# Kernel tuning notes

Hardware: AMD Instinct MI355X
Metric: run time of the kernel (lower is better)

The kernel has to match this reference:

```python
import jax, jax.numpy as jnp
import numpy as np

B, S, D = 8, 2048, 64
H = 128


def setup_inputs() -> dict:
    key = jax.random.key(0)
    k = jax.random.split(key, 5)
    X = jax.random.normal(k[0], (B, S, D), dtype=jnp.float32)
    Wi = jax.random.normal(k[1], (H, D), dtype=jnp.float32)          # init_layer weight, std=1
    bi = jax.random.normal(k[2], (H,), dtype=jnp.float32)            # init_layer bias, std=1
    Wa = jax.random.normal(k[3], (H * H, D + 1), dtype=jnp.float32) / jnp.sqrt(H)  # vf_A, std=1/sqrt(H)
    Wb = jax.random.normal(k[4], (H, D + 1), dtype=jnp.float32)      # vf_B, std=1
    return {"X": X, "Wi": Wi, "bi": bi, "Wa": Wa, "Wb": Wb}


def reference(X, Wi, bi, Wa, Wb):
    b, s, d = X.shape
    dt = 1.0 / (s - 1)
    # inp: time channel (constant dt) concatenated with scaled input -> [b, s, d+1]
    inp = jnp.concatenate([jnp.full((b, s, 1), dt, dtype=X.dtype), X * dt], axis=-1)
    y0 = X[:, 0] @ Wi.T + bi                       # [b, H]
    Bs = jnp.einsum('bsk,hk->bsh', inp[:, 1:], Wb)  # [b, s-1, H]

    def step(y, xs):
        inp_t, b_t = xs                            # [b, d+1], [b, H]
        A = (inp_t @ Wa.T).reshape(b, H, H)        # per-step transition matrix
        y_new = y + jnp.einsum('bij,bj->bi', A, y) + b_t
        return y_new, y_new

    xs = (jnp.swapaxes(inp[:, 1:], 0, 1), jnp.swapaxes(Bs, 0, 1))  # time-major
    _, ys_rest = jax.lax.scan(step, y0, xs)        # [s-1, b, H]
    ys = jnp.concatenate([y0[:, None, :], jnp.swapaxes(ys_rest, 0, 1)], axis=1)
    return ys
```

## Files before the change

kernel.cpp:

```cpp
#include <hip/hip_runtime.h>
#include <hip/hip_fp16.h>


typedef _Float16 h8 __attribute__((ext_vector_type(8)));
typedef float v4f __attribute__((ext_vector_type(4)));
typedef unsigned int uint;

constexpr int B_ = 8, S_ = 2048, D_ = 64, H_ = 128;
constexpr int T_ = S_ - 1;
constexpr int KD = D_ + 1;
constexpr float DTC = 1.0f / 2047.0f;
constexpr int L_ = 8;
constexpr int LSH = 3;
constexpr int NC = 256;

__global__ __launch_bounds__(256) void k_prep_wa(const float* __restrict__ Wa,
                                                 _Float16* __restrict__ Wa16B,
                                                 float* __restrict__ Wa0) {
  int idx = blockIdx.x * 256 + threadIdx.x;
  int r = idx >> 6, kk = idx & 63;
  int rt = r >> 4, n = r & 15;
  int kb = kk >> 5, q = (kk >> 3) & 3, jj = kk & 7;
  float v = Wa[(size_t)r * KD + 1 + kk];
  Wa16B[((((size_t)rt * 2 + kb) * 4 + q) * 16 + n) * 8 + jj] = (_Float16)v;
  if (kk == 0) Wa0[r] = Wa[(size_t)r * KD];
}

__global__ __launch_bounds__(256) void k_prep_x(const float* __restrict__ X,
                                                _Float16* __restrict__ Xs16) {
  int idx = blockIdx.x * 256 + threadIdx.x;
  int bt = idx >> 6, d = idx & 63;
  int b = bt / T_, s = bt - b * T_;
  Xs16[(size_t)bt * 64 + d] = (_Float16)(X[((size_t)b * S_ + s + 1) * D_ + d] * DTC);
}

__global__ __launch_bounds__(128) void k_y0(const float* __restrict__ X,
                                            const float* __restrict__ Wi,
                                            const float* __restrict__ bi,
                                            float* __restrict__ out,
                                            float* __restrict__ ybound) {
  int b = blockIdx.x, h = threadIdx.x;
  __shared__ float xs[D_];
  if (h < D_) xs[h] = X[(size_t)b * S_ * D_ + h];
  __syncthreads();
  float acc = bi[h];
  const float* wr = Wi + h * D_;
#pragma unroll 8
  for (int d = 0; d < D_; d++) acc += xs[d] * wr[d];
  out[(size_t)b * S_ * H_ + h] = acc;
  if (ybound) ybound[(size_t)(b * NC + 0) * H_ + h] = acc;
}

__global__ __launch_bounds__(256) void k_bs(const float* __restrict__ X,
                                            const float* __restrict__ Wb,
                                            float* __restrict__ Bs) {
  __shared__ float wb_s[H_ * KD];
  __shared__ float xs[16][D_ + 4];
  int tid = threadIdx.x;
  int bt0 = blockIdx.x * 16;
  for (int i = tid; i < H_ * KD; i += 256) wb_s[i] = Wb[i];
  for (int i = tid; i < 16 * D_; i += 256) {
    int sl = i >> 6, d = i & 63;
    int btg = bt0 + sl;
    float v = 0.f;
    if (btg < B_ * T_) {
      int b = btg / T_, s = btg - b * T_;
      v = X[((size_t)b * S_ + s + 1) * D_ + d] * DTC;
    }
    xs[sl][d] = v;
  }
  __syncthreads();
  int h = tid & 127, sh = tid >> 7;
  const float* wrow = &wb_s[h * KD];
  for (int u = 0; u < 8; u++) {
    int sl = sh * 8 + u;
    int btg = bt0 + sl;
    if (btg >= B_ * T_) break;
    float acc = wrow[0] * DTC;
#pragma unroll 8
    for (int d = 0; d < D_; d++) acc += xs[sl][d] * wrow[1 + d];
    Bs[(size_t)btg * H_ + h] = acc;
  }
}

__global__ __launch_bounds__(256) void k_amat(const _Float16* __restrict__ Xs16,
                                              const _Float16* __restrict__ Wa16B,
                                              const float* __restrict__ Wa0,
                                              _Float16* __restrict__ A_sl,
                                              int c0, int scShift) {
  __shared__ _Float16 sb[32 * 528];
  int tid = threadIdx.x;
  int w = tid >> 6, lane = tid & 63;
  int n = lane & 15, q = lane >> 4;
  int rowbase = blockIdx.x * 32;
  int SCm = ((1 << scShift) << LSH) - 1;

  h8 af[2][2];
#pragma unroll
  for (int mi = 0; mi < 2; mi++) {
    int sidx = rowbase + mi * 16 + n;
    int b = sidx >> (scShift + LSH);
    int rem = sidx & SCm;
    int cc = rem >> LSH, l = rem & (L_ - 1);
    int s = (c0 + cc) * L_ + l;
    if (s >= T_) s = T_ - 1;
    size_t btg = (size_t)b * T_ + s;
#pragma unroll
    for (int kb = 0; kb < 2; kb++)
      af[mi][kb] = *(const h8*)(Xs16 + btg * 64 + kb * 32 + q * 8);
  }

  v4f acc[2][8];
#pragma unroll
  for (int nj = 0; nj < 8; nj++) {
    int ct_g = blockIdx.y * 32 + w * 8 + nj;
    float binit = DTC * Wa0[ct_g * 16 + n];
    h8 bf0 = *(const h8*)(Wa16B + ((((size_t)ct_g * 2 + 0) * 4 + q) * 16 + n) * 8);
    h8 bf1 = *(const h8*)(Wa16B + ((((size_t)ct_g * 2 + 1) * 4 + q) * 16 + n) * 8);
#pragma unroll
    for (int mi = 0; mi < 2; mi++) {
      v4f a;
      a[0] = binit; a[1] = binit; a[2] = binit; a[3] = binit;
      a = __builtin_amdgcn_mfma_f32_16x16x32_f16(af[mi][0], bf0, a, 0, 0, 0);
      a = __builtin_amdgcn_mfma_f32_16x16x32_f16(af[mi][1], bf1, a, 0, 0, 0);
      acc[mi][nj] = a;
    }
  }
#pragma unroll
  for (int mi = 0; mi < 2; mi++)
#pragma unroll
    for (int nj = 0; nj < 8; nj++)
#pragma unroll
      for (int reg = 0; reg < 4; reg++)
        sb[(mi * 16 + q * 4 + reg) * 528 + w * 128 + ((nj * 16 + n) ^ (q * 16))] =
            (_Float16)acc[mi][nj][reg];
  __syncthreads();
#pragma unroll
  for (int it = 0; it < 8; it++) {
    int idx = tid + it * 256;
    int t = idx >> 6, u4 = idx & 63;
    int qt = (t >> 2) & 3;
    uint4 val = *(const uint4*)&sb[t * 528 + ((u4 * 8) ^ (qt * 16))];
    *(uint4*)(A_sl + (size_t)(rowbase + t) * 16384 + blockIdx.y * 512 + u4 * 8) = val;
  }
}

__global__ __launch_bounds__(256) void k_pair(const _Float16* __restrict__ A_sl,
                                              const float* __restrict__ Bs,
                                              _Float16* __restrict__ P1,
                                              float* __restrict__ v1,
                                              int c0, int scShift) {
  __shared__ _Float16 A0t[128 * 136];
  __shared__ float bs0[128], bs1[128];
  int tid = threadIdx.x;
  int w = tid >> 6, lane = tid & 63;
  int n = lane & 15, q = lane >> 4;
  int chunk = blockIdx.x >> 2;
  int j = blockIdx.x & 3;
  int SC = 1 << scShift;
  int b = chunk >> scShift;
  int cc = chunk & (SC - 1);
  int c = c0 + cc;
  int t0 = c * L_ + 2 * j;
  int valid1 = (t0 + 1) < T_;
  const _Float16* A0 = A_sl + ((size_t)chunk * L_ + 2 * j) * 16384;
  const _Float16* A1 = A0 + 16384;

#pragma unroll
  for (int it = 0; it < 8; it++) {
    int idx = tid + it * 256;
    int rowl = idx & 127, c8 = (idx >> 7) * 8;
    uint4 pk = *(const uint4*)(A0 + rowl * 128 + c8);
    const _Float16* hp = (const _Float16*)&pk;
#pragma unroll
    for (int cx = 0; cx < 8; cx++) A0t[(c8 + cx) * 136 + rowl] = hp[cx];
  }
  if (tid < 128) {
    size_t bt0 = (size_t)b * T_ + t0;
    bs0[tid] = Bs[bt0 * 128 + tid];
    bs1[tid] = valid1 ? Bs[(bt0 + 1) * 128 + tid] : 0.f;
  }
  h8 idE, idO;
#pragma unroll
  for (int jj = 0; jj < 8; jj++) {
    idE[jj] = (_Float16)((q * 8 + jj == n) ? 1.f : 0.f);
    idO[jj] = (_Float16)((q * 8 + jj == 16 + n) ? 1.f : 0.f);
  }
  h8 af[2][4];
  if (valid1) {
#pragma unroll
    for (int mi = 0; mi < 2; mi++)
#pragma unroll
      for (int kb = 0; kb < 4; kb++)
        af[mi][kb] = *(const h8*)(A1 + ((2 * w + mi) * 16 + n) * 128 + kb * 32 + q * 8);
  } else {
#pragma unroll
    for (int mi = 0; mi < 2; mi++)
#pragma unroll
      for (int kb = 0; kb < 4; kb++)
#pragma unroll
        for (int z = 0; z < 8; z++) af[mi][kb][z] = (_Float16)0;
  }
  __syncthreads();

  v4f acc[2][8];
#pragma unroll
  for (int mi = 0; mi < 2; mi++)
#pragma unroll
    for (int nj = 0; nj < 8; nj++)
#pragma unroll
      for (int reg = 0; reg < 4; reg++) acc[mi][nj][reg] = 0.f;

#pragma unroll
  for (int nj = 0; nj < 8; nj++) {
    h8 bfr[4];
#pragma unroll
    for (int kb = 0; kb < 4; kb++)
      bfr[kb] = *(const h8*)&A0t[(nj * 16 + n) * 136 + kb * 32 + q * 8];
#pragma unroll
    for (int mi = 0; mi < 2; mi++) {
#pragma unroll
      for (int kb = 0; kb < 4; kb++)
        acc[mi][nj] = __builtin_amdgcn_mfma_f32_16x16x32_f16(af[mi][kb], bfr[kb], acc[mi][nj], 0, 0, 0);
      acc[mi][nj] = __builtin_amdgcn_mfma_f32_16x16x32_f16(
          af[mi][nj >> 1], (nj & 1) ? idO : idE, acc[mi][nj], 0, 0, 0);
    }
  }

  float dv0 = 0.f, dv1 = 0.f;
#pragma unroll
  for (int kb = 0; kb < 4; kb++) {
    float4 p0 = *(const float4*)&bs0[kb * 32 + q * 8];
    float4 p1 = *(const float4*)&bs0[kb * 32 + q * 8 + 4];
    float vk[8] = {p0.x, p0.y, p0.z, p0.w, p1.x, p1.y, p1.z, p1.w};
#pragma unroll
    for (int jj = 0; jj < 8; jj++) {
      dv0 += (float)af[0][kb][jj] * vk[jj];
      dv1 += (float)af[1][kb][jj] * vk[jj];
    }
  }
  dv0 += __shfl_xor(dv0, 16); dv0 += __shfl_xor(dv0, 32);
  dv1 += __shfl_xor(dv1, 16); dv1 += __shfl_xor(dv1, 32);
  if (q == 0) {
    float* v1g = v1 + (size_t)blockIdx.x * 128;
    int r0v = 2 * w * 16 + n, r1v = (2 * w + 1) * 16 + n;
    v1g[r0v] = bs0[r0v] + bs1[r0v] + dv0;
    v1g[r1v] = bs0[r1v] + bs1[r1v] + dv1;
  }

#pragma unroll
  for (int mi = 0; mi < 2; mi++) {
    int row0 = (2 * w + mi) * 16 + q * 4;
#pragma unroll
    for (int nj = 0; nj < 8; nj++) {
      int col = nj * 16 + n;
      union { uint2 u; _Float16 h[4]; } m2;
      m2.u = *(const uint2*)&A0t[col * 136 + row0];
#pragma unroll
      for (int reg = 0; reg < 4; reg++) acc[mi][nj][reg] += (float)m2.h[reg];
    }
  }
  __syncthreads();
#pragma unroll
  for (int mi = 0; mi < 2; mi++) {
    int row0 = (2 * w + mi) * 16 + q * 4;
#pragma unroll
    for (int nj = 0; nj < 8; nj++) {
      int col = nj * 16 + n;
#pragma unroll
      for (int reg = 0; reg < 4; reg++)
        A0t[(row0 + reg) * 136 + col] = (_Float16)acc[mi][nj][reg];
    }
  }
  __syncthreads();
  _Float16* Pg = P1 + (size_t)blockIdx.x * 16384;
#pragma unroll
  for (int it = 0; it < 8; it++) {
    int idx = tid + it * 256;
    int rowl = idx >> 4, ch = idx & 15;
    uint4 val = *(const uint4*)&A0t[rowl * 136 + ch * 8];
    *(uint4*)(Pg + rowl * 128 + ch * 8) = val;
  }
}

__global__ __launch_bounds__(256) void k_comp4(const _Float16* __restrict__ in_map,
                                               const float* __restrict__ in_v,
                                               _Float16* __restrict__ out_map,
                                               float* __restrict__ out_v) {
  __shared__ _Float16 Dt[128 * 136];
  __shared__ float v32[128];
  int tid = threadIdx.x;
  int w = tid >> 6, lane = tid & 63;
  int n = lane & 15, q = lane >> 4;
  size_t nbase = (size_t)blockIdx.x * 4;

  const _Float16* P0 = in_map + nbase * 16384;
#pragma unroll
  for (int it = 0; it < 8; it++) {
    int idx = tid + it * 256;
    int rowl = idx & 127, c8 = (idx >> 7) * 8;
    uint4 pk = *(const uint4*)(P0 + rowl * 128 + c8);
    const _Float16* hp = (const _Float16*)&pk;
#pragma unroll
    for (int cx = 0; cx < 8; cx++) Dt[(c8 + cx) * 136 + rowl] = hp[cx];
  }
  if (tid < 128) v32[tid] = in_v[nbase * 128 + tid];
  h8 idE, idO;
#pragma unroll
  for (int jj = 0; jj < 8; jj++) {
    idE[jj] = (_Float16)((q * 8 + jj == n) ? 1.f : 0.f);
    idO[jj] = (_Float16)((q * 8 + jj == 16 + n) ? 1.f : 0.f);
  }
  __syncthreads();

  v4f acc[2][8];
#pragma unroll
  for (int mi = 0; mi < 2; mi++) {
    int row0 = (2 * w + mi) * 16 + q * 4;
#pragma unroll
    for (int nj = 0; nj < 8; nj++) {
      int col = nj * 16 + n;
      union { uint2 u; _Float16 h[4]; } m2;
      m2.u = *(const uint2*)&Dt[col * 136 + row0];
#pragma unroll
      for (int reg = 0; reg < 4; reg++) acc[mi][nj][reg] = (float)m2.h[reg];
    }
  }

  int r0 = 2 * w * 16 + n, r1 = r0 + 16;
  for (int j = 1; j < 4; j++) {
    const _Float16* Pj = in_map + (nbase + j) * 16384;
    h8 af[2][4];
#pragma unroll
    for (int mi = 0; mi < 2; mi++)
#pragma unroll
      for (int kb = 0; kb < 4; kb++)
        af[mi][kb] = *(const h8*)(Pj + ((2 * w + mi) * 16 + n) * 128 + kb * 32 + q * 8);
#pragma unroll
    for (int nj = 0; nj < 8; nj++) {
      h8 bfr[4];
#pragma unroll
      for (int kb = 0; kb < 4; kb++)
        bfr[kb] = *(const h8*)&Dt[(nj * 16 + n) * 136 + kb * 32 + q * 8];
#pragma unroll
      for (int mi = 0; mi < 2; mi++) {
#pragma unroll
        for (int kb = 0; kb < 4; kb++)
          acc[mi][nj] = __builtin_amdgcn_mfma_f32_16x16x32_f16(af[mi][kb], bfr[kb], acc[mi][nj], 0, 0, 0);
        acc[mi][nj] = __builtin_amdgcn_mfma_f32_16x16x32_f16(
            af[mi][nj >> 1], (nj & 1) ? idO : idE, acc[mi][nj], 0, 0, 0);
      }
    }
    float dv0 = 0.f, dv1 = 0.f;
#pragma unroll
    for (int kb = 0; kb < 4; kb++) {
      float4 p0 = *(const float4*)&v32[kb * 32 + q * 8];
      float4 p1 = *(const float4*)&v32[kb * 32 + q * 8 + 4];
      float vk[8] = {p0.x, p0.y, p0.z, p0.w, p1.x, p1.y, p1.z, p1.w};
#pragma unroll
      for (int jj = 0; jj < 8; jj++) {
        dv0 += (float)af[0][kb][jj] * vk[jj];
        dv1 += (float)af[1][kb][jj] * vk[jj];
      }
    }
    dv0 += __shfl_xor(dv0, 16); dv0 += __shfl_xor(dv0, 32);
    dv1 += __shfl_xor(dv1, 16); dv1 += __shfl_xor(dv1, 32);
    float vold0 = v32[r0], vold1 = v32[r1];
    float vj0 = 0.f, vj1 = 0.f;
    if (q == 0) {
      vj0 = in_v[(nbase + j) * 128 + r0];
      vj1 = in_v[(nbase + j) * 128 + r1];
    }
    __syncthreads();
#pragma unroll
    for (int mi = 0; mi < 2; mi++) {
      int row0 = (2 * w + mi) * 16 + q * 4;
#pragma unroll
      for (int nj = 0; nj < 8; nj++) {
        int col = nj * 16 + n;
        union { _Float16 h[4]; uint2 u; } pk;
#pragma unroll
        for (int reg = 0; reg < 4; reg++) pk.h[reg] = (_Float16)acc[mi][nj][reg];
        *(uint2*)&Dt[col * 136 + row0] = pk.u;
      }
    }
    if (q == 0) {
      v32[r0] = vold0 + dv0 + vj0;
      v32[r1] = vold1 + dv1 + vj1;
    }
    __syncthreads();
  }
#pragma unroll
  for (int mi = 0; mi < 2; mi++) {
    int row0 = (2 * w + mi) * 16 + q * 4;
#pragma unroll
    for (int nj = 0; nj < 8; nj++) {
      int col = nj * 16 + n;
#pragma unroll
      for (int reg = 0; reg < 4; reg++)
        Dt[(row0 + reg) * 136 + col] = (_Float16)acc[mi][nj][reg];
    }
  }
  __syncthreads();
  _Float16* og = out_map + (size_t)blockIdx.x * 16384;
#pragma unroll
  for (int it = 0; it < 8; it++) {
    int idx = tid + it * 256;
    int rowl = idx >> 4, ch = idx & 15;
    uint4 val = *(const uint4*)&Dt[rowl * 136 + ch * 8];
    *(uint4*)(og + rowl * 128 + ch * 8) = val;
  }
  if (tid < 128) out_v[(size_t)blockIdx.x * 128 + tid] = v32[tid];
}

__global__ __launch_bounds__(256) void k_chainsuper(const _Float16* __restrict__ Sr,
                                                    const float* __restrict__ sv,
                                                    float* __restrict__ yb,
                                                    int c0, int scShift) {
  int b = blockIdx.x, tid = threadIdx.x;
  int NS = 1 << (scShift - 2);
  int i = tid >> 1, hh = tid & 1;
  __shared__ float ybuf[128];
  __shared__ float red[128];
  if (tid < 128) ybuf[tid] = yb[(size_t)(b * NC + c0) * 128 + tid];
  __syncthreads();

  uint4 arA[8], arB[8];
  float svA, svB;

#define LOADS(ar, svv, s)                                                            \
  {                                                                                  \
    const uint4* p = (const uint4*)(Sr + (size_t)(b * NS + (s)) * 16384 + i * 128 + hh * 64); \
    _Pragma("unroll")                                                                \
    for (int u = 0; u < 8; u++) ar[u] = p[u];                                        \
    svv = sv[(size_t)(b * NS + (s)) * 128 + i];                                      \
  }

#define STEPS(ar, svv, s)                                                            \
  {                                                                                  \
    float pt = 0.f;                                                                  \
    _Pragma("unroll")                                                                \
    for (int u = 0; u < 8; u++) {                                                    \
      union { uint4 v; _Float16 h[8]; } wv; wv.v = ar[u];                            \
      _Pragma("unroll")                                                              \
      for (int k = 0; k < 8; k++) pt += (float)wv.h[k] * ybuf[hh * 64 + u * 8 + k];  \
    }                                                                                \
    if (hh) red[i] = pt;                                                             \
    __syncthreads();                                                                 \
    if (!hh) {                                                                       \
      float yn = ybuf[i] + pt + red[i] + svv;                                        \
      int cg = c0 + 4 * ((s) + 1);                                                   \
      if (cg < NC) yb[(size_t)(b * NC + cg) * 128 + i] = yn;                         \
      ybuf[i] = yn;                                                                  \
    }                                                                                \
    __syncthreads();                                                                 \
  }

  LOADS(arA, svA, 0);
  int s = 0;
  for (; s + 1 < NS; s += 2) {
    LOADS(arB, svB, s + 1);
    STEPS(arA, svA, s);
    if (s + 2 < NS) LOADS(arA, svA, s + 2);
    STEPS(arB, svB, s + 1);
  }
  if (s < NS) STEPS(arA, svA, s);
#undef LOADS
#undef STEPS
}

__global__ __launch_bounds__(256) void k_fill(const _Float16* __restrict__ Mr,
                                              const float* __restrict__ vch,
                                              float* __restrict__ yb,
                                              int c0, int scShift) {
  int tid = threadIdx.x;
  int NS = 1 << (scShift - 2);
  int b = blockIdx.x >> (scShift - 2);
  int s = blockIdx.x & (NS - 1);
  int i = tid >> 1, hh = tid & 1;
  __shared__ float ybuf[128];
  __shared__ float red[128];
  if (tid < 128) ybuf[tid] = yb[(size_t)(b * NC + c0 + 4 * s) * 128 + tid];
  __syncthreads();
  size_t node0 = ((size_t)b << scShift) + 4 * s;

  uint4 arA[8], arB[8];
  float vvA, vvB;

#define LOADF(ar, vv, k)                                                             \
  {                                                                                  \
    const uint4* p = (const uint4*)(Mr + (node0 + (k)) * 16384 + i * 128 + hh * 64); \
    _Pragma("unroll")                                                                \
    for (int u = 0; u < 8; u++) ar[u] = p[u];                                        \
    vv = vch[(node0 + (k)) * 128 + i];                                               \
  }

#define STEPF(ar, vv, k)                                                             \
  {                                                                                  \
    float pt = 0.f;                                                                  \
    _Pragma("unroll")                                                                \
    for (int u = 0; u < 8; u++) {                                                    \
      union { uint4 v; _Float16 h[8]; } wv; wv.v = ar[u];                            \
      _Pragma("unroll")                                                              \
      for (int kk = 0; kk < 8; kk++) pt += (float)wv.h[kk] * ybuf[hh * 64 + u * 8 + kk]; \
    }                                                                                \
    if (hh) red[i] = pt;                                                             \
    __syncthreads();                                                                 \
    if (!hh) {                                                                       \
      float yn = ybuf[i] + pt + red[i] + vv;                                         \
      yb[(size_t)(b * NC + c0 + 4 * s + (k) + 1) * 128 + i] = yn;                    \
      ybuf[i] = yn;                                                                  \
    }                                                                                \
    __syncthreads();                                                                 \
  }

  LOADF(arA, vvA, 0);
  LOADF(arB, vvB, 1);
  STEPF(arA, vvA, 0);
  LOADF(arA, vvA, 2);
  STEPF(arB, vvB, 1);
  STEPF(arA, vvA, 2);
#undef LOADF
#undef STEPF
}

__global__ __launch_bounds__(256) void k_emit(const _Float16* __restrict__ A_sl,
                                              const float* __restrict__ Bs,
                                              const float* __restrict__ yb,
                                              float* __restrict__ out,
                                              int c0, int scShift) {
  int tid = threadIdx.x;
  int SC = 1 << scShift;
  int b = blockIdx.x >> scShift;
  int cc = blockIdx.x & (SC - 1);
  int c = c0 + cc;
  int i = tid >> 1, hh = tid & 1;
  __shared__ float ybuf[128];
  __shared__ float red[128];
  if (tid < 128) ybuf[tid] = yb[(size_t)(b * NC + c) * 128 + tid];
  __syncthreads();
  int nst = min(L_, T_ - c * L_);
  size_t sidx0 = (size_t)blockIdx.x * L_;
  size_t btb = (size_t)b * T_ + c * L_;

  uint4 arA[8], arB[8];
  float bsA, bsB;

#define LOADR(ar, bsv, l)                                                            \
  {                                                                                  \
    const uint4* p = (const uint4*)(A_sl + (sidx0 + (l)) * 16384 + i * 128 + hh * 64); \
    _Pragma("unroll")                                                                \
    for (int u = 0; u < 8; u++) ar[u] = p[u];                                        \
    bsv = Bs[(btb + (l)) * 128 + i];                                                 \
  }

#define STEPE(ar, bsv, l)                                                            \
  {                                                                                  \
    float pt = 0.f;                                                                  \
    _Pragma("unroll")                                                                \
    for (int u = 0; u < 8; u++) {                                                    \
      union { uint4 v; _Float16 h[8]; } wv; wv.v = ar[u];                            \
      _Pragma("unroll")                                                              \
      for (int k = 0; k < 8; k++) pt += (float)wv.h[k] * ybuf[hh * 64 + u * 8 + k];  \
    }                                                                                \
    if (hh) red[i] = pt;                                                             \
    __syncthreads();                                                                 \
    if (!hh) {                                                                       \
      float yn = ybuf[i] + pt + red[i] + bsv;                                        \
      out[((size_t)b * S_ + (size_t)(c * L_ + (l) + 1)) * 128 + i] = yn;             \
      ybuf[i] = yn;                                                                  \
    }                                                                                \
    __syncthreads();                                                                 \
  }

  LOADR(arA, bsA, 0);
  for (int l = 0; l < nst; l += 2) {
    if (l + 1 < nst) LOADR(arB, bsB, l + 1);
    STEPE(arA, bsA, l);
    if (l + 2 < nst) LOADR(arA, bsA, l + 2);
    if (l + 1 < nst) STEPE(arB, bsB, l + 1);
  }
#undef LOADR
#undef STEPE
}

__global__ __launch_bounds__(256) void k_seq(const float* __restrict__ X,
                                             const float* __restrict__ Wa,
                                             const float* __restrict__ Wb,
                                             float* __restrict__ out) {
  int b = blockIdx.x, tid = threadIdx.x;
  int i = tid >> 1, hh = tid & 1;
  __shared__ float y[H_], red[H_], xs[D_], bts[H_];
  if (tid < H_) y[tid] = out[(size_t)b * S_ * H_ + tid];
  __syncthreads();
  for (int t = 1; t < S_; t++) {
    if (tid < D_) xs[tid] = X[((size_t)b * S_ + t) * D_ + tid] * DTC;
    __syncthreads();
    if (tid < H_) {
      const float* wr = Wb + tid * KD;
      float acc = wr[0] * DTC;
#pragma unroll 8
      for (int d = 0; d < D_; d++) acc += xs[d] * wr[1 + d];
      bts[tid] = acc;
    }
    float part = 0.f;
    const float* yhalf = &y[hh * 64];
    for (int j = 0; j < 64; j++) {
      const float* wr = Wa + ((size_t)(i * H_) + hh * 64 + j) * KD;
      float a = wr[0] * DTC;
#pragma unroll 8
      for (int d = 0; d < D_; d++) a += xs[d] * wr[1 + d];
      part += a * yhalf[j];
    }
    if (hh) red[i] = part;
    __syncthreads();
    if (!hh) {
      float yn = y[i] + part + red[i] + bts[i];
      out[((size_t)b * S_ + t) * H_ + i] = yn;
      y[i] = yn;
    }
    __syncthreads();
  }
}

extern "C" void kernel_launch(void* const* d_in, const int* in_sizes, int n_in,
                              void* d_out, int out_size, void* d_ws, size_t ws_size,
                              hipStream_t stream) {
  (void)in_sizes; (void)n_in; (void)out_size;
  const float* X  = (const float*)d_in[0];
  const float* Wi = (const float*)d_in[1];
  const float* bi = (const float*)d_in[2];
  const float* Wa = (const float*)d_in[3];
  const float* Wb = (const float*)d_in[4];
  float* out = (float*)d_out;
  char* ws = (char*)d_ws;

  size_t off = 0;
  auto alloc = [&](size_t bytes) { size_t o = off; off = (off + bytes + 255) & ~(size_t)255; return o; };
  size_t oBs  = alloc((size_t)B_ * T_ * 128 * 4);
  size_t oYb  = alloc((size_t)B_ * NC * 128 * 4);
  size_t oWaB = alloc((size_t)64 * 16384 * 2);
  size_t oWa0 = alloc((size_t)16384 * 4);
  size_t oXs  = alloc((size_t)B_ * T_ * 64 * 2);
  size_t fixed = off;

  const size_t APC  = (size_t)B_ * L_ * 16384 * 2;
  const size_t P1PC = (size_t)B_ * 4 * 16384 * 2;
  const size_t V1PC = (size_t)B_ * 4 * 128 * 4;
  const size_t MRPC = (size_t)B_ * 16384 * 2;
  const size_t VCPC = (size_t)B_ * 128 * 4;
  const size_t SRPC = (size_t)B_ * 16384 * 2 / 4;
  const size_t SVPC = (size_t)B_ * 128;
  const size_t PER_SC = APC + P1PC + V1PC + MRPC + VCPC + SRPC + SVPC + 7 * 256;

  int SC = 0;
  if (ws_size > fixed) {
    size_t avail = ws_size - fixed;
    SC = 64;
    while (SC >= 4 && (size_t)SC * PER_SC > avail) SC >>= 1;
    if (SC < 4) SC = 0;
  }
  if (SC < 4) {
    k_y0<<<B_, 128, 0, stream>>>(X, Wi, bi, out, nullptr);
    k_seq<<<B_, 256, 0, stream>>>(X, Wa, Wb, out);
    return;
  }
  int scShift = __builtin_ctz(SC);

  size_t oMr = alloc((size_t)SC * MRPC);
  size_t oVc = alloc((size_t)SC * VCPC);
  size_t oP1 = alloc((size_t)SC * P1PC);
  size_t oV1 = alloc((size_t)SC * V1PC);
  size_t oSr = alloc((size_t)SC * SRPC);
  size_t oSv = alloc((size_t)SC * SVPC);
  size_t oA  = alloc((size_t)SC * APC);

  float*    Bs    = (float*)(ws + oBs);
  float*    yb    = (float*)(ws + oYb);
  _Float16* Wa16B = (_Float16*)(ws + oWaB);
  float*    Wa0   = (float*)(ws + oWa0);
  _Float16* Xs16  = (_Float16*)(ws + oXs);
  _Float16* Mr    = (_Float16*)(ws + oMr);
  float*    vch   = (float*)(ws + oVc);
  _Float16* P1    = (_Float16*)(ws + oP1);
  float*    v1    = (float*)(ws + oV1);
  _Float16* Sr    = (_Float16*)(ws + oSr);
  float*    sv    = (float*)(ws + oSv);
  _Float16* A_sl  = (_Float16*)(ws + oA);

  k_prep_wa<<<4096, 256, 0, stream>>>(Wa, Wa16B, Wa0);
  k_prep_x<<<4094, 256, 0, stream>>>(X, Xs16);
  k_y0<<<B_, 128, 0, stream>>>(X, Wi, bi, out, yb);
  k_bs<<<(B_ * T_ + 15) / 16, 256, 0, stream>>>(X, Wb, Bs);

  int nslices = NC / SC;
  int chunks = B_ * SC;
  int amat_gx = (B_ * SC * L_) / 32;
  for (int si = 0; si < nslices; si++) {
    int c0 = si * SC;
    k_amat<<<dim3(amat_gx, 32), 256, 0, stream>>>(Xs16, Wa16B, Wa0, A_sl, c0, scShift);
    k_pair<<<4 * chunks, 256, 0, stream>>>(A_sl, Bs, P1, v1, c0, scShift);
    k_comp4<<<chunks, 256, 0, stream>>>(P1, v1, Mr, vch);
    k_comp4<<<chunks / 4, 256, 0, stream>>>(Mr, vch, Sr, sv);
    k_chainsuper<<<B_, 256, 0, stream>>>(Sr, sv, yb, c0, scShift);
    k_fill<<<chunks / 4, 256, 0, stream>>>(Mr, vch, yb, c0, scShift);
    k_emit<<<chunks, 256, 0, stream>>>(A_sl, Bs, yb, out, c0, scShift);
  }
}
```

Baseline: 706.8 us.

## Fuse pair and first compose into a sequential per-chunk map kernel

```diff
diff --git a/kernel.cpp b/kernel.cpp
--- a/kernel.cpp
+++ b/kernel.cpp
@@ -145,109 +145,45 @@
   }
 }
 
-__global__ __launch_bounds__(256) void k_pair(const _Float16* __restrict__ A_sl,
-                                              const float* __restrict__ Bs,
-                                              _Float16* __restrict__ P1,
-                                              float* __restrict__ v1,
-                                              int c0, int scShift) {
-  __shared__ _Float16 A0t[128 * 136];
-  __shared__ float bs0[128], bs1[128];
+__global__ __launch_bounds__(256) void k_chunkmap(const _Float16* __restrict__ A_sl,
+                                                  const float* __restrict__ Bs,
+                                                  _Float16* __restrict__ Mr,
+                                                  float* __restrict__ vch,
+                                                  int c0, int scShift) {
+  __shared__ _Float16 Dt[128 * 136];
+  __shared__ float v32[128];
   int tid = threadIdx.x;
   int w = tid >> 6, lane = tid & 63;
   int n = lane & 15, q = lane >> 4;
-  int chunk = blockIdx.x >> 2;
-  int j = blockIdx.x & 3;
+  int chunk = blockIdx.x;
   int SC = 1 << scShift;
   int b = chunk >> scShift;
   int cc = chunk & (SC - 1);
   int c = c0 + cc;
-  int t0 = c * L_ + 2 * j;
-  int valid1 = (t0 + 1) < T_;
-  const _Float16* A0 = A_sl + ((size_t)chunk * L_ + 2 * j) * 16384;
-  const _Float16* A1 = A0 + 16384;
+  int sbase = c * L_;
+  int nsteps = min(L_, T_ - sbase);
+  const _Float16* Abase = A_sl + (size_t)chunk * L_ * 16384;
+  size_t btb = (size_t)b * T_ + sbase;
 
 #pragma unroll
   for (int it = 0; it < 8; it++) {
     int idx = tid + it * 256;
     int rowl = idx & 127, c8 = (idx >> 7) * 8;
-    uint4 pk = *(const uint4*)(A0 + rowl * 128 + c8);
+    uint4 pk = *(const uint4*)(Abase + rowl * 128 + c8);
     const _Float16* hp = (const _Float16*)&pk;
 #pragma unroll
-    for (int cx = 0; cx < 8; cx++) A0t[(c8 + cx) * 136 + rowl] = hp[cx];
-  }
-  if (tid < 128) {
-    size_t bt0 = (size_t)b * T_ + t0;
-    bs0[tid] = Bs[bt0 * 128 + tid];
-    bs1[tid] = valid1 ? Bs[(bt0 + 1) * 128 + tid] : 0.f;
-  }
+    for (int cx = 0; cx < 8; cx++) Dt[(c8 + cx) * 136 + rowl] = hp[cx];
+  }
+  if (tid < 128) v32[tid] = Bs[btb * 128 + tid];
   h8 idE, idO;
 #pragma unroll
   for (int jj = 0; jj < 8; jj++) {
     idE[jj] = (_Float16)((q * 8 + jj == n) ? 1.f : 0.f);
     idO[jj] = (_Float16)((q * 8 + jj == 16 + n) ? 1.f : 0.f);
   }
-  h8 af[2][4];
-  if (valid1) {
-#pragma unroll
-    for (int mi = 0; mi < 2; mi++)
-#pragma unroll
-      for (int kb = 0; kb < 4; kb++)
-        af[mi][kb] = *(const h8*)(A1 + ((2 * w + mi) * 16 + n) * 128 + kb * 32 + q * 8);
-  } else {
-#pragma unroll
-    for (int mi = 0; mi < 2; mi++)
-#pragma unroll
-      for (int kb = 0; kb < 4; kb++)
-#pragma unroll
-        for (int z = 0; z < 8; z++) af[mi][kb][z] = (_Float16)0;
-  }
   __syncthreads();
 
   v4f acc[2][8];
-#pragma unroll
-  for (int mi = 0; mi < 2; mi++)
-#pragma unroll
-    for (int nj = 0; nj < 8; nj++)
-#pragma unroll
-      for (int reg = 0; reg < 4; reg++) acc[mi][nj][reg] = 0.f;
-
-#pragma unroll
-  for (int nj = 0; nj < 8; nj++) {
-    h8 bfr[4];
-#pragma unroll
-    for (int kb = 0; kb < 4; kb++)
-      bfr[kb] = *(const h8*)&A0t[(nj * 16 + n) * 136 + kb * 32 + q * 8];
-#pragma unroll
-    for (int mi = 0; mi < 2; mi++) {
-#pragma unroll
-      for (int kb = 0; kb < 4; kb++)
-        acc[mi][nj] = __builtin_amdgcn_mfma_f32_16x16x32_f16(af[mi][kb], bfr[kb], acc[mi][nj], 0, 0, 0);
-      acc[mi][nj] = __builtin_amdgcn_mfma_f32_16x16x32_f16(
-          af[mi][nj >> 1], (nj & 1) ? idO : idE, acc[mi][nj], 0, 0, 0);
-    }
-  }
-
-  float dv0 = 0.f, dv1 = 0.f;
-#pragma unroll
-  for (int kb = 0; kb < 4; kb++) {
-    float4 p0 = *(const float4*)&bs0[kb * 32 + q * 8];
-    float4 p1 = *(const float4*)&bs0[kb * 32 + q * 8 + 4];
-    float vk[8] = {p0.x, p0.y, p0.z, p0.w, p1.x, p1.y, p1.z, p1.w};
-#pragma unroll
-    for (int jj = 0; jj < 8; jj++) {
-      dv0 += (float)af[0][kb][jj] * vk[jj];
-      dv1 += (float)af[1][kb][jj] * vk[jj];
-    }
-  }
-  dv0 += __shfl_xor(dv0, 16); dv0 += __shfl_xor(dv0, 32);
-  dv1 += __shfl_xor(dv1, 16); dv1 += __shfl_xor(dv1, 32);
-  if (q == 0) {
-    float* v1g = v1 + (size_t)blockIdx.x * 128;
-    int r0v = 2 * w * 16 + n, r1v = (2 * w + 1) * 16 + n;
-    v1g[r0v] = bs0[r0v] + bs1[r0v] + dv0;
-    v1g[r1v] = bs0[r1v] + bs1[r1v] + dv1;
-  }
-
 #pragma unroll
   for (int mi = 0; mi < 2; mi++) {
     int row0 = (2 * w + mi) * 16 + q * 4;
@@ -255,12 +191,92 @@
     for (int nj = 0; nj < 8; nj++) {
       int col = nj * 16 + n;
       union { uint2 u; _Float16 h[4]; } m2;
-      m2.u = *(const uint2*)&A0t[col * 136 + row0];
-#pragma unroll
-      for (int reg = 0; reg < 4; reg++) acc[mi][nj][reg] += (float)m2.h[reg];
-    }
-  }
-  __syncthreads();
+      m2.u = *(const uint2*)&Dt[col * 136 + row0];
+#pragma unroll
+      for (int reg = 0; reg < 4; reg++) acc[mi][nj][reg] = (float)m2.h[reg];
+    }
+  }
+
+  int r0 = 2 * w * 16 + n, r1 = r0 + 16;
+  h8 afA[2][4], afB[2][4];
+
+#define LOADA(dst, l)                                                                \
+  {                                                                                  \
+    const _Float16* Ag = Abase + (size_t)(l) * 16384;                                \
+    _Pragma("unroll")                                                                \
+    for (int mi = 0; mi < 2; mi++)                                                   \
+      _Pragma("unroll")                                                              \
+      for (int kb = 0; kb < 4; kb++)                                                 \
+        dst[mi][kb] = *(const h8*)(Ag + ((2 * w + mi) * 16 + n) * 128 + kb * 32 + q * 8); \
+  }
+
+#define STEPQ(af, l)                                                                 \
+  {                                                                                  \
+    _Pragma("unroll")                                                                \
+    for (int nj = 0; nj < 8; nj++) {                                                 \
+      h8 bfr[4];                                                                     \
+      _Pragma("unroll")                                                              \
+      for (int kb = 0; kb < 4; kb++)                                                 \
+        bfr[kb] = *(const h8*)&Dt[(nj * 16 + n) * 136 + kb * 32 + q * 8];            \
+      _Pragma("unroll")                                                              \
+      for (int mi = 0; mi < 2; mi++) {                                               \
+        _Pragma("unroll")                                                            \
+        for (int kb = 0; kb < 4; kb++)                                               \
+          acc[mi][nj] = __builtin_amdgcn_mfma_f32_16x16x32_f16(af[mi][kb], bfr[kb], acc[mi][nj], 0, 0, 0); \
+        acc[mi][nj] = __builtin_amdgcn_mfma_f32_16x16x32_f16(                        \
+            af[mi][nj >> 1], (nj & 1) ? idO : idE, acc[mi][nj], 0, 0, 0);            \
+      }                                                                              \
+    }                                                                                \
+    float dv0 = 0.f, dv1 = 0.f;                                                      \
+    _Pragma("unroll")                                                                \
+    for (int kb = 0; kb < 4; kb++) {                                                 \
+      float4 p0 = *(const float4*)&v32[kb * 32 + q * 8];                             \
+      float4 p1 = *(const float4*)&v32[kb * 32 + q * 8 + 4];                         \
+      float vk[8] = {p0.x, p0.y, p0.z, p0.w, p1.x, p1.y, p1.z, p1.w};                \
+      _Pragma("unroll")                                                              \
+      for (int jj = 0; jj < 8; jj++) {                                               \
+        dv0 += (float)af[0][kb][jj] * vk[jj];                                        \
+        dv1 += (float)af[1][kb][jj] * vk[jj];                                        \
+      }                                                                              \
+    }                                                                                \
+    dv0 += __shfl_xor(dv0, 16); dv0 += __shfl_xor(dv0, 32);                          \
+    dv1 += __shfl_xor(dv1, 16); dv1 += __shfl_xor(dv1, 32);                          \
+    float vold0 = v32[r0], vold1 = v32[r1];                                          \
+    float bs0 = 0.f, bs1 = 0.f;                                                      \
+    if (q == 0) {                                                                    \
+      bs0 = Bs[(btb + (l)) * 128 + r0];                                              \
+      bs1 = Bs[(btb + (l)) * 128 + r1];                                              \
+    }                                                                                \
+    __syncthreads();                                                                 \
+    _Pragma("unroll")                                                                \
+    for (int mi = 0; mi < 2; mi++) {                                                 \
+      int row0 = (2 * w + mi) * 16 + q * 4;                                          \
+      _Pragma("unroll")                                                              \
+      for (int nj = 0; nj < 8; nj++) {                                               \
+        int col = nj * 16 + n;                                                       \
+        union { _Float16 h[4]; uint2 u; } pk;                                        \
+        _Pragma("unroll")                                                            \
+        for (int reg = 0; reg < 4; reg++) pk.h[reg] = (_Float16)acc[mi][nj][reg];    \
+        *(uint2*)&Dt[col * 136 + row0] = pk.u;                                       \
+      }                                                                              \
+    }                                                                                \
+    if (q == 0) {                                                                    \
+      v32[r0] = vold0 + dv0 + bs0;                                                   \
+      v32[r1] = vold1 + dv1 + bs1;                                                   \
+    }                                                                                \
+    __syncthreads();                                                                 \
+  }
+
+  LOADA(afA, 1);
+  for (int l = 1; l < nsteps; l += 2) {
+    if (l + 1 < nsteps) LOADA(afB, l + 1);
+    STEPQ(afA, l);
+    if (l + 2 < nsteps) LOADA(afA, l + 2);
+    if (l + 1 < nsteps) STEPQ(afB, l + 1);
+  }
+#undef LOADA
+#undef STEPQ
+
 #pragma unroll
   for (int mi = 0; mi < 2; mi++) {
     int row0 = (2 * w + mi) * 16 + q * 4;
@@ -269,18 +285,19 @@
       int col = nj * 16 + n;
 #pragma unroll
       for (int reg = 0; reg < 4; reg++)
-        A0t[(row0 + reg) * 136 + col] = (_Float16)acc[mi][nj][reg];
-    }
-  }
-  __syncthreads();
-  _Float16* Pg = P1 + (size_t)blockIdx.x * 16384;
+        Dt[(row0 + reg) * 136 + col] = (_Float16)acc[mi][nj][reg];
+    }
+  }
+  __syncthreads();
+  _Float16* og = Mr + (size_t)chunk * 16384;
 #pragma unroll
   for (int it = 0; it < 8; it++) {
     int idx = tid + it * 256;
     int rowl = idx >> 4, ch = idx & 15;
-    uint4 val = *(const uint4*)&A0t[rowl * 136 + ch * 8];
-    *(uint4*)(Pg + rowl * 128 + ch * 8) = val;
-  }
+    uint4 val = *(const uint4*)&Dt[rowl * 136 + ch * 8];
+    *(uint4*)(og + rowl * 128 + ch * 8) = val;
+  }
+  if (tid < 128) vch[(size_t)chunk * 128 + tid] = v32[tid];
 }
 
 __global__ __launch_bounds__(256) void k_comp4(const _Float16* __restrict__ in_map,
@@ -645,13 +662,11 @@
   size_t fixed = off;
 
   const size_t APC  = (size_t)B_ * L_ * 16384 * 2;
-  const size_t P1PC = (size_t)B_ * 4 * 16384 * 2;
-  const size_t V1PC = (size_t)B_ * 4 * 128 * 4;
   const size_t MRPC = (size_t)B_ * 16384 * 2;
   const size_t VCPC = (size_t)B_ * 128 * 4;
   const size_t SRPC = (size_t)B_ * 16384 * 2 / 4;
   const size_t SVPC = (size_t)B_ * 128;
-  const size_t PER_SC = APC + P1PC + V1PC + MRPC + VCPC + SRPC + SVPC + 7 * 256;
+  const size_t PER_SC = APC + MRPC + VCPC + SRPC + SVPC + 5 * 256;
 
   int SC = 0;
   if (ws_size > fixed) {
@@ -669,8 +684,6 @@
 
   size_t oMr = alloc((size_t)SC * MRPC);
   size_t oVc = alloc((size_t)SC * VCPC);
-  size_t oP1 = alloc((size_t)SC * P1PC);
-  size_t oV1 = alloc((size_t)SC * V1PC);
   size_t oSr = alloc((size_t)SC * SRPC);
   size_t oSv = alloc((size_t)SC * SVPC);
   size_t oA  = alloc((size_t)SC * APC);
@@ -682,8 +695,6 @@
   _Float16* Xs16  = (_Float16*)(ws + oXs);
   _Float16* Mr    = (_Float16*)(ws + oMr);
   float*    vch   = (float*)(ws + oVc);
-  _Float16* P1    = (_Float16*)(ws + oP1);
-  float*    v1    = (float*)(ws + oV1);
   _Float16* Sr    = (_Float16*)(ws + oSr);
   float*    sv    = (float*)(ws + oSv);
   _Float16* A_sl  = (_Float16*)(ws + oA);
@@ -699,8 +710,7 @@
   for (int si = 0; si < nslices; si++) {
     int c0 = si * SC;
     k_amat<<<dim3(amat_gx, 32), 256, 0, stream>>>(Xs16, Wa16B, Wa0, A_sl, c0, scShift);
-    k_pair<<<4 * chunks, 256, 0, stream>>>(A_sl, Bs, P1, v1, c0, scShift);
-    k_comp4<<<chunks, 256, 0, stream>>>(P1, v1, Mr, vch);
+    k_chunkmap<<<chunks, 256, 0, stream>>>(A_sl, Bs, Mr, vch, c0, scShift);
     k_comp4<<<chunks / 4, 256, 0, stream>>>(Mr, vch, Sr, sv);
     k_chainsuper<<<B_, 256, 0, stream>>>(Sr, sv, yb, c0, scShift);
     k_fill<<<chunks / 4, 256, 0, stream>>>(Mr, vch, yb, c0, scShift);
```

Measured after the change: 616.1 us. 12.8% less time.
